# Kernel optimization log

Hardware: AMD Instinct MI355X
Metric: run time of the kernel (lower is better)

## Reference

```python
import jax, jax.numpy as jnp
import numpy as np


def _retain(o1, others, W, bias):
    # o1: (b, s, h); others: (b, 4, s, h); W: (h, h); bias: (1,)
    q = o1 @ W                                        # (b, s, h)
    scores = jnp.einsum('bih,bkjh->bijk', q, others) + bias[0]  # (b, s1, s2, 4)
    w = jax.nn.softmax(scores, axis=-1)               # softmax over the 4 options
    # weight[:, :, :, k] @ option_k summed over k
    return jnp.einsum('bijk,bkjh->bih', w, others)


def setup_inputs() -> dict:
    key = jax.random.key(0)
    ks = jax.random.split(key, 7)
    b, s, h = 32, 256, 1024
    opts = {f'option{i+1}': jax.random.normal(ks[i], (b, s, h), dtype=jnp.float32)
            for i in range(5)}
    W = 0.02 * jax.random.normal(ks[5], (h, h), dtype=jnp.float32)
    bias = 0.02 * jax.random.normal(ks[6], (1,), dtype=jnp.float32)
    return {**opts, 'W': W, 'bias': bias}


def reference(option1, option2, option3, option4, option5, W, bias):
    opts = [option1, option2, option3, option4, option5]
    total = None
    for i in range(5):
        others = jnp.stack([opts[j] for j in range(5) if j != i], axis=1)  # (b,4,s,h)
        r = _retain(opts[i], others, W, bias)
        total = r if total is None else total + r
    return total / 2.0
```

## Files before the change

kernel.cpp:

```cpp
#include <hip/hip_runtime.h>
#include <hip/hip_bf16.h>
#include <stdint.h>


#define BB 32
#define SS 256
#define HH 1024

typedef __attribute__((ext_vector_type(4))) float f32x4;
typedef __attribute__((ext_vector_type(8))) __bf16 bf16x8;
typedef __attribute__((ext_vector_type(4))) __bf16 bf16x4;

__device__ constexpr int PAIR(int i, int n) { return i * 4 + (n > i ? n - 1 : n); }

__device__ __forceinline__ void gload_lds16(const void* g, void* l) {
  __builtin_amdgcn_global_load_lds((const __attribute__((address_space(1))) void*)g,
                                   (__attribute__((address_space(3))) void*)l, 16, 0, 0);
}

__global__ void canary(float* out, float v) { out[0] = v; }

__global__ __launch_bounds__(256) void cast_all(
    const float* p0, const float* p1, const float* p2, const float* p3, const float* p4,
    __bf16* __restrict__ dst)
{
  int m = blockIdx.x >> 12;
  long off = ((long)(blockIdx.x & 4095) * 256 + threadIdx.x) * 8;
  const float* src = m == 0 ? p0 : m == 1 ? p1 : m == 2 ? p2 : m == 3 ? p3 : p4;
  float4 v0 = *(const float4*)(src + off);
  float4 v1 = *(const float4*)(src + off + 4);
  bf16x8 h;
  h[0] = (__bf16)v0.x; h[1] = (__bf16)v0.y; h[2] = (__bf16)v0.z; h[3] = (__bf16)v0.w;
  h[4] = (__bf16)v1.x; h[5] = (__bf16)v1.y; h[6] = (__bf16)v1.z; h[7] = (__bf16)v1.w;
  *(bf16x8*)(dst + (long)m * BB * SS * HH + off) = h;
}

__global__ __launch_bounds__(256) void cast_trW(const float* __restrict__ src,
                                                __bf16* __restrict__ dstT)
{
  __shared__ __bf16 tile[64][72];
  int ct = blockIdx.x & 15, rt = blockIdx.x >> 4;
  const float* s = src + (long)(rt * 64) * 1024 + ct * 64;
  int t = threadIdx.x;
#pragma unroll
  for (int p = 0; p < 4; p++) {
    int c = t + p * 256;
    int row = c >> 4, c4 = c & 15;
    float4 v = *(const float4*)(s + (long)row * 1024 + c4 * 4);
    bf16x4 h;
    h[0] = (__bf16)v.x; h[1] = (__bf16)v.y; h[2] = (__bf16)v.z; h[3] = (__bf16)v.w;
    *(bf16x4*)&tile[row][c4 * 4] = h;
  }
  __syncthreads();
#pragma unroll
  for (int p = 0; p < 4; p++) {
    int c = t + p * 256;
    int hr = c >> 4, s4 = c & 15;
    bf16x4 h;
    h[0] = tile[s4 * 4 + 0][hr];
    h[1] = tile[s4 * 4 + 1][hr];
    h[2] = tile[s4 * 4 + 2][hr];
    h[3] = tile[s4 * 4 + 3][hr];
    *(bf16x4*)(dstT + (long)(ct * 64 + hr) * 1024 + rt * 64 + s4 * 4) = h;
  }
}

__global__ __launch_bounds__(256, 3) void qgemm_b16(
    const __bf16* __restrict__ A, const __bf16* __restrict__ Bt, __bf16* __restrict__ C)
{
  __shared__ __align__(16) char ldsb[3 * 16384];
  int lin = blockIdx.x;
  int xcd = lin & 7, idx = lin >> 3;
  int rt = xcd * 40 + (idx >> 3), ct = idx & 7;
  int t = threadIdx.x, l = t & 63, w = t >> 6;
  int wm = w >> 1, wn = w & 1;
  f32x4 acc[4][4] = {};

  const char *gA0, *gA1, *gB0, *gB1;
  {
    int c0 = t, c1 = t + 256;
    int r0 = c0 >> 2, h0 = (c0 & 3) ^ ((c0 >> 3) & 3);
    int r1 = c1 >> 2, h1 = (c1 & 3) ^ ((c1 >> 3) & 3);
    gA0 = (const char*)(A + (long)(rt * 128 + r0) * 1024 + h0 * 8);
    gA1 = (const char*)(A + (long)(rt * 128 + r1) * 1024 + h1 * 8);
    gB0 = (const char*)(Bt + (long)(ct * 128 + r0) * 1024 + h0 * 8);
    gB1 = (const char*)(Bt + (long)(ct * 128 + r1) * 1024 + h1 * 8);
  }
  int dst0 = w * 1024, dst1 = (w + 4) * 1024;

#define STAGE(BUF)                                                \
  {                                                               \
    char* base = ldsb + (BUF) * 16384;                            \
    gload_lds16(gA0, base + dst0); gA0 += 64;                     \
    gload_lds16(gA1, base + dst1); gA1 += 64;                     \
    gload_lds16(gB0, base + 8192 + dst0); gB0 += 64;              \
    gload_lds16(gB1, base + 8192 + dst1); gB1 += 64;              \
  }

  int lr = l & 15, sl = l >> 4;
  int swz = (sl ^ ((lr >> 1) & 3)) * 16;
  int aoff = (wm * 64 + lr) * 64 + swz;
  int boff = 8192 + (wn * 64 + lr) * 64 + swz;

#define COMPUTE(BUF)                                                                   \
  {                                                                                    \
    const char* base = ldsb + (BUF) * 16384;                                           \
    bf16x8 af[4], bfr[4];                                                              \
    _Pragma("unroll") for (int i = 0; i < 4; i++) {                                    \
      af[i]  = *(const bf16x8*)(base + aoff + i * 1024);                               \
      bfr[i] = *(const bf16x8*)(base + boff + i * 1024);                               \
    }                                                                                  \
    __builtin_amdgcn_s_setprio(1);                                                     \
    _Pragma("unroll") for (int i = 0; i < 4; i++)                                      \
      _Pragma("unroll") for (int j = 0; j < 4; j++)                                    \
        acc[i][j] = __builtin_amdgcn_mfma_f32_16x16x32_bf16(af[i], bfr[j],             \
                                                            acc[i][j], 0, 0, 0);       \
    __builtin_amdgcn_s_setprio(0);                                                     \
  }

#define STEP(CUR, STG)                                          \
  asm volatile("s_waitcnt vmcnt(4)" ::: "memory");              \
  __builtin_amdgcn_s_barrier();                                 \
  STAGE(STG);                                                   \
  COMPUTE(CUR);

  STAGE(0)
  STAGE(1)
  for (int it = 0; it < 10; it++) {
    STEP(0, 2)
    STEP(1, 0)
    STEP(2, 1)
  }
  asm volatile("s_waitcnt vmcnt(4)" ::: "memory");
  __builtin_amdgcn_s_barrier();
  COMPUTE(0)
  asm volatile("s_waitcnt vmcnt(0)" ::: "memory");
  __builtin_amdgcn_s_barrier();
  COMPUTE(1)
#undef STEP
#undef COMPUTE
#undef STAGE

#pragma unroll
  for (int i = 0; i < 4; i++) {
    long mrow = (long)rt * 128 + wm * 64 + i * 16 + ((l >> 4) << 2);
#pragma unroll
    for (int j = 0; j < 4; j++) {
      int n = ct * 128 + wn * 64 + j * 16 + (l & 15);
#pragma unroll
      for (int r = 0; r < 4; r++)
        C[(mrow + r) * 1024 + n] = (__bf16)acc[i][j][r];
    }
  }
}

__global__ __launch_bounds__(256, 2) void gram_b16(
    const __bf16* __restrict__ Q, const __bf16* __restrict__ O, __bf16* __restrict__ V)
{
  __shared__ __align__(16) char ldsb[3 * 20480];
  int bid = blockIdx.x;
  int xcd = bid & 7, idx = bid >> 3;
  int b = xcd * 4 + (idx >> 6);
  int rem = idx & 63;
  int s1t = rem >> 3, s2t = rem & 7;
  int t = threadIdx.x, l = t & 63, w = t >> 6;
  int pr = w >> 1, pc = w & 1;
  f32x4 acc[20] = {};

  long qrow0 = (long)b * SS + s1t * 32;
  long orow0 = (long)b * SS + s2t * 32;
  int slog = (l & 3) ^ ((l >> 3) & 3);
  const char* gp0; const char* gp1; const char* gp2; const char* gp3; const char* gp4;
#define GP_INIT(GP, P)                                                                \
  {                                                                                   \
    int g = 4 * (P) + w;                                                              \
    int isQ = g < 10;                                                                 \
    int gg = isQ ? g : g - 10;                                                        \
    long row = (long)(gg >> 1) * (BB * SS) + (isQ ? qrow0 : orow0) + (g & 1) * 16 +   \
               (l >> 2);                                                              \
    GP = (const char*)((isQ ? Q : O) + row * HH + slog * 8);                          \
  }
  GP_INIT(gp0, 0) GP_INIT(gp1, 1) GP_INIT(gp2, 2) GP_INIT(gp3, 3) GP_INIT(gp4, 4)
#undef GP_INIT
  int g0 = w, g1 = 4 + w, g2 = 8 + w, g3 = 12 + w, g4 = 16 + w;

#define STAGE(BB_)                                                      \
  {                                                                     \
    char* base = ldsb + (BB_) * 20480;                                  \
    gload_lds16(gp0, base + g0 * 1024); gp0 += 64;                      \
    gload_lds16(gp1, base + g1 * 1024); gp1 += 64;                      \
    gload_lds16(gp2, base + g2 * 1024); gp2 += 64;                      \
    gload_lds16(gp3, base + g3 * 1024); gp3 += 64;                      \
    gload_lds16(gp4, base + g4 * 1024); gp4 += 64;                      \
  }

  int lr = l & 15, sl = l >> 4;
  int swz = (sl ^ ((lr >> 1) & 3)) * 16;
  int qoff = (pr * 16 + lr) * 64 + swz;
  int ooff = 10240 + (pc * 16 + lr) * 64 + swz;

#define COMPUTE(BB_)                                                                   \
  {                                                                                    \
    const char* base = ldsb + (BB_) * 20480;                                           \
    bf16x8 qf[5], of[5];                                                               \
    _Pragma("unroll") for (int m = 0; m < 5; m++) {                                    \
      qf[m] = *(const bf16x8*)(base + m * 2048 + qoff);                                \
      of[m] = *(const bf16x8*)(base + m * 2048 + ooff);                                \
    }                                                                                  \
    __builtin_amdgcn_s_setprio(1);                                                     \
    _Pragma("unroll") for (int i = 0; i < 5; i++) {                                    \
      _Pragma("unroll") for (int n = 0; n < 5; n++) {                                  \
        if (n != i)                                                                    \
          acc[PAIR(i, n)] =                                                            \
              __builtin_amdgcn_mfma_f32_16x16x32_bf16(qf[i], of[n], acc[PAIR(i, n)],   \
                                                      0, 0, 0);                        \
      }                                                                                \
    }                                                                                  \
    __builtin_amdgcn_s_setprio(0);                                                     \
  }

#define STEP(CUR, STG)                                          \
  asm volatile("s_waitcnt vmcnt(5)" ::: "memory");              \
  __builtin_amdgcn_s_barrier();                                 \
  STAGE(STG);                                                   \
  COMPUTE(CUR);

  STAGE(0)
  STAGE(1)
  for (int it = 0; it < 10; it++) {
    STEP(0, 2)
    STEP(1, 0)
    STEP(2, 1)
  }
  asm volatile("s_waitcnt vmcnt(5)" ::: "memory");
  __builtin_amdgcn_s_barrier();
  COMPUTE(0)
  asm volatile("s_waitcnt vmcnt(0)" ::: "memory");
  __builtin_amdgcn_s_barrier();
  COMPUTE(1)
#undef STEP
#undef COMPUTE
#undef STAGE

  int s1g = s1t * 32 + pr * 16 + ((l >> 4) << 2);
  int s2g = s2t * 32 + pc * 16 + (l & 15);
#pragma unroll
  for (int r = 0; r < 4; r++) {
    float vacc[5] = {0.f, 0.f, 0.f, 0.f, 0.f};
#pragma unroll
    for (int i = 0; i < 5; i++) {
      float gg[5];
      float mx = -3.0e38f;
#pragma unroll
      for (int n = 0; n < 5; n++)
        if (n != i) { gg[n] = acc[PAIR(i, n)][r]; mx = fmaxf(mx, gg[n]); }
      float ee[5], ssum = 0.f;
#pragma unroll
      for (int n = 0; n < 5; n++)
        if (n != i) { ee[n] = __expf(gg[n] - mx); ssum += ee[n]; }
      float inv = 1.0f / ssum;
#pragma unroll
      for (int n = 0; n < 5; n++)
        if (n != i) vacc[n] += ee[n] * inv;
    }
#pragma unroll
    for (int n = 0; n < 5; n++)
      V[((long)(n * 32 + b) * 256 + s1g + r) * 256 + s2g] = (__bf16)vacc[n];
  }
}

__global__ __launch_bounds__(256) void pvgemm(
    const __bf16* __restrict__ Vb, const __bf16* __restrict__ Obf, float* __restrict__ out)
{
  __shared__ __bf16 smA[128][40];
  __shared__ __bf16 smB[128][40];
  int bid = blockIdx.x;
  int b = bid >> 4, s1t = (bid >> 3) & 1, ht = bid & 7;
  int t = threadIdx.x, l = t & 63, w = t >> 6;
  int wm = w >> 1, wn = w & 1;
  f32x4 acc[4][4] = {};
#pragma unroll
  for (int n = 0; n < 5; n++) {
    const __bf16* On = Obf + (long)n * BB * SS * HH;
    for (int st2 = 0; st2 < 8; st2++) {
      int s20 = st2 * 32;
#pragma unroll
      for (int p = 0; p < 2; p++) {
        int c = t + p * 256;
        int row = c >> 2, sl = c & 3;
        *(bf16x8*)&smA[row][sl * 8] =
            *(const bf16x8*)(Vb + (long)(n * BB + b) * SS * SS + (long)(s1t * 128 + row) * SS +
                             s20 + sl * 8);
      }
      {
        int h4 = (t & 31) * 4, s2q = (t >> 5) * 4;
        const __bf16* src = On + ((long)b * 256 + s20 + s2q) * 1024 + ht * 128 + h4;
        bf16x4 v0 = *(const bf16x4*)(src);
        bf16x4 v1 = *(const bf16x4*)(src + 1024);
        bf16x4 v2 = *(const bf16x4*)(src + 2048);
        bf16x4 v3 = *(const bf16x4*)(src + 3072);
        bf16x4 c0, c1, c2, c3;
        c0[0] = v0[0]; c0[1] = v1[0]; c0[2] = v2[0]; c0[3] = v3[0];
        c1[0] = v0[1]; c1[1] = v1[1]; c1[2] = v2[1]; c1[3] = v3[1];
        c2[0] = v0[2]; c2[1] = v1[2]; c2[2] = v2[2]; c2[3] = v3[2];
        c3[0] = v0[3]; c3[1] = v1[3]; c3[2] = v2[3]; c3[3] = v3[3];
        *(bf16x4*)&smB[h4 + 0][s2q] = c0;
        *(bf16x4*)&smB[h4 + 1][s2q] = c1;
        *(bf16x4*)&smB[h4 + 2][s2q] = c2;
        *(bf16x4*)&smB[h4 + 3][s2q] = c3;
      }
      __syncthreads();
      bf16x8 af[4], bfr[4];
      int sl = l >> 4, lr = l & 15;
#pragma unroll
      for (int i = 0; i < 4; i++) {
        af[i]  = *(const bf16x8*)&smA[wm * 64 + i * 16 + lr][sl * 8];
        bfr[i] = *(const bf16x8*)&smB[wn * 64 + i * 16 + lr][sl * 8];
      }
#pragma unroll
      for (int i = 0; i < 4; i++)
#pragma unroll
        for (int j = 0; j < 4; j++)
          acc[i][j] = __builtin_amdgcn_mfma_f32_16x16x32_bf16(af[i], bfr[j], acc[i][j], 0, 0, 0);
      __syncthreads();
    }
  }
#pragma unroll
  for (int i = 0; i < 4; i++) {
    int m = s1t * 128 + wm * 64 + i * 16 + ((l >> 4) << 2);
#pragma unroll
    for (int j = 0; j < 4; j++) {
      int n = ht * 128 + wn * 64 + j * 16 + (l & 15);
#pragma unroll
      for (int r = 0; r < 4; r++)
        out[(long)(b * SS + m + r) * HH + n] = 0.5f * acc[i][j][r];
    }
  }
}

extern "C" void kernel_launch(void* const* d_in, const int* in_sizes, int n_in,
                              void* d_out, int out_size, void* d_ws, size_t ws_size,
                              hipStream_t stream)
{
  const size_t SZ_W = (size_t)HH * HH * 2;
  const size_t SZ_Q = (size_t)5 * BB * SS * HH * 2;
  const size_t SZ_V = (size_t)5 * BB * SS * SS * 2;
  const size_t SZ_O = (size_t)5 * BB * SS * HH * 2;
  const size_t NEED = SZ_W + SZ_Q + SZ_V + SZ_O;
  if (ws_size < NEED) {
    canary<<<1, 1, 0, stream>>>((float*)d_out, (float)(ws_size >> 20));
    return;
  }
  char* ws = (char*)d_ws;
  __bf16* Wt  = (__bf16*)ws;
  __bf16* Qb  = (__bf16*)(ws + SZ_W);
  __bf16* Vb  = (__bf16*)(ws + SZ_W + SZ_Q);
  __bf16* Obf = (__bf16*)(ws + SZ_W + SZ_Q + SZ_V);
  const float* o0 = (const float*)d_in[0];
  const float* o1 = (const float*)d_in[1];
  const float* o2 = (const float*)d_in[2];
  const float* o3 = (const float*)d_in[3];
  const float* o4 = (const float*)d_in[4];

  cast_trW<<<256, 256, 0, stream>>>((const float*)d_in[5], Wt);
  cast_all<<<5 * 4096, 256, 0, stream>>>(o0, o1, o2, o3, o4, Obf);
  qgemm_b16<<<2560, 256, 0, stream>>>(Obf, Wt, Qb);
  gram_b16<<<2048, 256, 0, stream>>>(Qb, Obf, Vb);
  pvgemm<<<512, 256, 0, stream>>>(Vb, Obf, (float*)d_out);
}
```

Before: 294.9 us.

## Enlarge Q-GEMM tiles to 256x256 with 512-thread blocks

The Q = O·W GEMM kernel moves from 128x128 tiles with 256 threads to 256x256 tiles with 512 threads (8 waves, each computing 128x64). The grid shrinks from 2560 to 640 blocks and LDS per stage doubles to 32KB. The aim is to halve global/L2 traffic per output element and raise MFMA work per LDS read. In exchange it uses more registers (32 accumulators per wave), fewer resident blocks, and a coarser grid that may load-balance worse across CUs.

```diff
diff --git a/kernel.cpp b/kernel.cpp
--- a/kernel.cpp
+++ b/kernel.cpp
@@ -65,53 +65,56 @@
   }
 }
 
-__global__ __launch_bounds__(256, 3) void qgemm_b16(
+__global__ __launch_bounds__(512, 2) void qgemm256(
     const __bf16* __restrict__ A, const __bf16* __restrict__ Bt, __bf16* __restrict__ C)
 {
-  __shared__ __align__(16) char ldsb[3 * 16384];
+  __shared__ __align__(16) char ldsb[3 * 32768];
   int lin = blockIdx.x;
   int xcd = lin & 7, idx = lin >> 3;
-  int rt = xcd * 40 + (idx >> 3), ct = idx & 7;
+  int rt = xcd * 20 + (idx >> 2), ct = idx & 3;
   int t = threadIdx.x, l = t & 63, w = t >> 6;
-  int wm = w >> 1, wn = w & 1;
-  f32x4 acc[4][4] = {};
-
-  const char *gA0, *gA1, *gB0, *gB1;
-  {
-    int c0 = t, c1 = t + 256;
-    int r0 = c0 >> 2, h0 = (c0 & 3) ^ ((c0 >> 3) & 3);
-    int r1 = c1 >> 2, h1 = (c1 & 3) ^ ((c1 >> 3) & 3);
-    gA0 = (const char*)(A + (long)(rt * 128 + r0) * 1024 + h0 * 8);
-    gA1 = (const char*)(A + (long)(rt * 128 + r1) * 1024 + h1 * 8);
-    gB0 = (const char*)(Bt + (long)(ct * 128 + r0) * 1024 + h0 * 8);
-    gB1 = (const char*)(Bt + (long)(ct * 128 + r1) * 1024 + h1 * 8);
-  }
-  int dst0 = w * 1024, dst1 = (w + 4) * 1024;
+  int wr = w >> 2, wc = w & 3;
+  f32x4 acc[8][4] = {};
+
+  const char* gp[4];
+  int dstp[4];
+#pragma unroll
+  for (int p = 0; p < 4; p++) {
+    int c = t + 512 * p;
+    int ch = c & 1023;
+    int row = ch >> 2;
+    int sl2 = (ch & 3) ^ ((ch >> 3) & 3);
+    if (p < 2)
+      gp[p] = (const char*)(A + (long)(rt * 256 + row) * 1024 + sl2 * 8);
+    else
+      gp[p] = (const char*)(Bt + (long)(ct * 256 + row) * 1024 + sl2 * 8);
+    dstp[p] = (w + 8 * p) << 10;
+  }
 
 #define STAGE(BUF)                                                \
   {                                                               \
-    char* base = ldsb + (BUF) * 16384;                            \
-    gload_lds16(gA0, base + dst0); gA0 += 64;                     \
-    gload_lds16(gA1, base + dst1); gA1 += 64;                     \
-    gload_lds16(gB0, base + 8192 + dst0); gB0 += 64;              \
-    gload_lds16(gB1, base + 8192 + dst1); gB1 += 64;              \
+    char* base = ldsb + (BUF) * 32768;                            \
+    _Pragma("unroll") for (int p = 0; p < 4; p++) {               \
+      gload_lds16(gp[p], base + dstp[p]);                         \
+      gp[p] += 64;                                                \
+    }                                                             \
   }
 
   int lr = l & 15, sl = l >> 4;
   int swz = (sl ^ ((lr >> 1) & 3)) * 16;
-  int aoff = (wm * 64 + lr) * 64 + swz;
-  int boff = 8192 + (wn * 64 + lr) * 64 + swz;
+  int aoff = (wr * 128 + lr) * 64 + swz;
+  int boff = 16384 + (wc * 64 + lr) * 64 + swz;
 
 #define COMPUTE(BUF)                                                                   \
   {                                                                                    \
-    const char* base = ldsb + (BUF) * 16384;                                           \
-    bf16x8 af[4], bfr[4];                                                              \
-    _Pragma("unroll") for (int i = 0; i < 4; i++) {                                    \
-      af[i]  = *(const bf16x8*)(base + aoff + i * 1024);                               \
-      bfr[i] = *(const bf16x8*)(base + boff + i * 1024);                               \
-    }                                                                                  \
+    const char* base = ldsb + (BUF) * 32768;                                           \
+    bf16x8 af[8], bfr[4];                                                              \
+    _Pragma("unroll") for (int i = 0; i < 8; i++)                                      \
+      af[i] = *(const bf16x8*)(base + aoff + i * 1024);                                \
+    _Pragma("unroll") for (int j = 0; j < 4; j++)                                      \
+      bfr[j] = *(const bf16x8*)(base + boff + j * 1024);                               \
     __builtin_amdgcn_s_setprio(1);                                                     \
-    _Pragma("unroll") for (int i = 0; i < 4; i++)                                      \
+    _Pragma("unroll") for (int i = 0; i < 8; i++)                                      \
       _Pragma("unroll") for (int j = 0; j < 4; j++)                                    \
         acc[i][j] = __builtin_amdgcn_mfma_f32_16x16x32_bf16(af[i], bfr[j],             \
                                                             acc[i][j], 0, 0, 0);       \
@@ -142,11 +145,11 @@
 #undef STAGE
 
 #pragma unroll
-  for (int i = 0; i < 4; i++) {
-    long mrow = (long)rt * 128 + wm * 64 + i * 16 + ((l >> 4) << 2);
+  for (int i = 0; i < 8; i++) {
+    long mrow = (long)rt * 256 + wr * 128 + i * 16 + (sl << 2);
 #pragma unroll
     for (int j = 0; j < 4; j++) {
-      int n = ct * 128 + wn * 64 + j * 16 + (l & 15);
+      int n = ct * 256 + wc * 64 + j * 16 + lr;
 #pragma unroll
       for (int r = 0; r < 4; r++)
         C[(mrow + r) * 1024 + n] = (__bf16)acc[i][j][r];
@@ -364,7 +367,7 @@
 
   cast_trW<<<256, 256, 0, stream>>>((const float*)d_in[5], Wt);
   cast_all<<<5 * 4096, 256, 0, stream>>>(o0, o1, o2, o3, o4, Obf);
-  qgemm_b16<<<2560, 256, 0, stream>>>(Obf, Wt, Qb);
+  qgemm256<<<640, 512, 0, stream>>>(Obf, Wt, Qb);
   gram_b16<<<2048, 256, 0, stream>>>(Qb, Obf, Vb);
   pvgemm<<<512, 256, 0, stream>>>(Vb, Obf, (float*)d_out);
 }
```

Result: faster. 280.3 us (-4.9%).
